# Performance work log

Measured on AMD Instinct MI355X. Metric: run time of the kernel, lower is better.

Reference implementation:

```python
import jax, jax.numpy as jnp
import numpy as np

N_NODES = 100000
N_EDGES = 1600000
IN_CH = 128
HIDDEN = 64
HEADS = 4
C = HIDDEN // HEADS  # per-head channels = 16
NEG_SLOPE = 0.2  # PyG GATConv default leaky_relu slope


def setup_inputs() -> dict:
    key = jax.random.key(0)
    ks = jax.random.split(key, 12)
    x = jax.random.normal(ks[0], (N_NODES, IN_CH), dtype=jnp.float32)
    edge_index = jax.random.randint(ks[1], (2, N_EDGES), 0, N_NODES, dtype=jnp.int64)
    s = 0.1
    params = {
        'w1': jax.random.normal(ks[2], (HIDDEN, IN_CH), dtype=jnp.float32) * s,
        'a_src1': jax.random.normal(ks[3], (HEADS, C), dtype=jnp.float32) * s,
        'a_dst1': jax.random.normal(ks[4], (HEADS, C), dtype=jnp.float32) * s,
        'b1': jax.random.normal(ks[5], (HIDDEN,), dtype=jnp.float32) * s,
        'w2': jax.random.normal(ks[6], (HIDDEN, HIDDEN), dtype=jnp.float32) * s,
        'a_src2': jax.random.normal(ks[7], (HEADS, C), dtype=jnp.float32) * s,
        'a_dst2': jax.random.normal(ks[8], (HEADS, C), dtype=jnp.float32) * s,
        'b2': jax.random.normal(ks[9], (HIDDEN,), dtype=jnp.float32) * s,
        'fc_w': jax.random.normal(ks[10], (1, HIDDEN), dtype=jnp.float32) * s,
        'fc_b': jax.random.normal(ks[11], (1,), dtype=jnp.float32) * s,
    }
    return {'x': x, 'edge_index': edge_index, **params}


def _gat_layer(x, src, dst, W, a_src, a_dst, b):
    # x: [N, F_in]; src/dst: [E'] (self-loops already appended)
    N = x.shape[0]
    h = (x @ W.T).reshape(N, HEADS, C)                      # [N, H, C]
    e_src = jnp.einsum('nhc,hc->nh', h, a_src)              # [N, H]
    e_dst = jnp.einsum('nhc,hc->nh', h, a_dst)              # [N, H]
    alpha = jax.nn.leaky_relu(e_src[src] + e_dst[dst], NEG_SLOPE)  # [E', H]
    # segment softmax over incoming edges of each dst node
    amax = jax.ops.segment_max(alpha, dst, num_segments=N)  # [N, H]
    alpha = jnp.exp(alpha - amax[dst])
    denom = jax.ops.segment_sum(alpha, dst, num_segments=N)
    alpha = alpha / (denom[dst] + 1e-16)
    msg = h[src] * alpha[:, :, None]                        # [E', H, C]
    out = jax.ops.segment_sum(msg, dst, num_segments=N)     # [N, H, C]
    return out.reshape(N, HEADS * C) + b


def _forward(x, edge_index, w1, a_src1, a_dst1, b1, w2, a_src2, a_dst2, b2, fc_w, fc_b):
    N = x.shape[0]
    loops = jnp.arange(N, dtype=edge_index.dtype)
    src = jnp.concatenate([edge_index[0], loops])  # PyG GATConv add_self_loops=True
    dst = jnp.concatenate([edge_index[1], loops])
    x = jax.nn.elu(_gat_layer(x, src, dst, w1, a_src1, a_dst1, b1))
    x = jax.nn.elu(_gat_layer(x, src, dst, w2, a_src2, a_dst2, b2))
    return x @ fc_w.T + fc_b  # [N, 1]


def reference(x, edge_index, w1, a_src1, a_dst1, b1, w2, a_src2, a_dst2, b2, fc_w, fc_b):
    return _forward(x, edge_index, w1, a_src1, a_dst1, b1, w2, a_src2, a_dst2, b2, fc_w, fc_b)
```

## Files before the change

kernel.cpp:

```cpp
#include <hip/hip_runtime.h>
#include <hip/hip_fp16.h>
#include <math.h>

#define NEG_SLOPE 0.2f
#define BSH 8
#define CAPB 6144

__device__ __forceinline__ float lrelu(float x) { return x > 0.f ? x : NEG_SLOPE * x; }

template <typename TIn>
__device__ __forceinline__ float4 ld4(const TIn* p);
template <>
__device__ __forceinline__ float4 ld4<float>(const float* p) { return *(const float4*)p; }
template <>
__device__ __forceinline__ float4 ld4<__half>(const __half* p) {
    uint2 u = *(const uint2*)p;
    union { unsigned v; __half h[2]; } a, b;
    a.v = u.x; b.v = u.y;
    return make_float4(__half2float(a.h[0]), __half2float(a.h[1]),
                       __half2float(b.h[0]), __half2float(b.h[1]));
}

template <int K, typename TIn>
__device__ __forceinline__ void gemm_body(const TIn* __restrict__ x,
                                          const float* __restrict__ W,
                                          const float* __restrict__ a_src,
                                          const float* __restrict__ a_dst,
                                          unsigned short* __restrict__ h_f16,
                                          float* __restrict__ es,
                                          float* __restrict__ ed,
                                          int N, int bid) {
    constexpr int CK = 32;
    __shared__ float xs[CK][68];
    __shared__ float ws[CK][68];
    const int tid = threadIdx.x;
    const int n0 = bid * 64;
    const int tx = tid & 15, ty = tid >> 4;

    float acc[4][4] = {};

    for (int k0 = 0; k0 < K; k0 += CK) {
#pragma unroll
        for (int i = 0; i < 2; ++i) {
            int slot = tid + i * 256;
            int nl = slot >> 3;
            int kq = slot & 7;
            int n = n0 + nl;
            float4 v = (n < N) ? ld4<TIn>(x + (size_t)n * K + k0 + kq * 4)
                               : make_float4(0.f, 0.f, 0.f, 0.f);
            xs[kq * 4 + 0][nl] = v.x; xs[kq * 4 + 1][nl] = v.y;
            xs[kq * 4 + 2][nl] = v.z; xs[kq * 4 + 3][nl] = v.w;
            float4 wv = *(const float4*)(W + (size_t)nl * K + k0 + kq * 4);
            ws[kq * 4 + 0][nl] = wv.x; ws[kq * 4 + 1][nl] = wv.y;
            ws[kq * 4 + 2][nl] = wv.z; ws[kq * 4 + 3][nl] = wv.w;
        }
        __syncthreads();
#pragma unroll
        for (int k = 0; k < CK; ++k) {
            float4 xv = *(const float4*)(&xs[k][ty * 4]);
            float4 wv = *(const float4*)(&ws[k][tx * 4]);
            float xa[4] = {xv.x, xv.y, xv.z, xv.w};
            float wa[4] = {wv.x, wv.y, wv.z, wv.w};
#pragma unroll
            for (int a = 0; a < 4; ++a)
#pragma unroll
                for (int c = 0; c < 4; ++c)
                    acc[a][c] += xa[a] * wa[c];
        }
        __syncthreads();
    }

    const float4 av = *(const float4*)(a_src + tx * 4);
    const float4 dv = *(const float4*)(a_dst + tx * 4);
#pragma unroll
    for (int a = 0; a < 4; ++a) {
        int n = n0 + ty * 4 + a;
        uint2 pk;
        pk.x = (unsigned)__half_as_ushort(__float2half_rn(acc[a][0])) |
               ((unsigned)__half_as_ushort(__float2half_rn(acc[a][1])) << 16);
        pk.y = (unsigned)__half_as_ushort(__float2half_rn(acc[a][2])) |
               ((unsigned)__half_as_ushort(__float2half_rn(acc[a][3])) << 16);
        if (n < N)
            *(uint2*)(h_f16 + (size_t)n * 64 + tx * 4) = pk;
        float e1 = acc[a][0] * av.x + acc[a][1] * av.y + acc[a][2] * av.z + acc[a][3] * av.w;
        float e2 = acc[a][0] * dv.x + acc[a][1] * dv.y + acc[a][2] * dv.z + acc[a][3] * dv.w;
        e1 += __shfl_xor(e1, 1, 64); e2 += __shfl_xor(e2, 1, 64);
        e1 += __shfl_xor(e1, 2, 64); e2 += __shfl_xor(e2, 2, 64);
        if ((tx & 3) == 0 && n < N) {
            es[(size_t)n * 4 + (tx >> 2)] = e1;
            ed[(size_t)n * 4 + (tx >> 2)] = e2;
        }
    }
}

template <int K>
__global__ __launch_bounds__(256) void gemm1_hist(const float* __restrict__ x,
                                                  const float* __restrict__ W,
                                                  const float* __restrict__ a_src,
                                                  const float* __restrict__ a_dst,
                                                  unsigned short* __restrict__ h_f16,
                                                  float* __restrict__ es,
                                                  float* __restrict__ ed, int N,
                                                  const int* __restrict__ dst,
                                                  int* __restrict__ hist_g,
                                                  int E, int Etot, int NBUCK, int nIter,
                                                  int NH) {
    if ((int)blockIdx.x < NH) {
        __shared__ int hist[512];
        int blk = blockIdx.x, tid = threadIdx.x;
        for (int i = tid; i < NBUCK; i += 256) hist[i] = 0;
        __syncthreads();
        int base = blk * nIter * 256;
        for (int i = 0; i < nIter; ++i) {
            int e = base + i * 256 + tid;
            if (e < Etot) {
                int d = (e < E) ? dst[e] : e - E;
                atomicAdd(&hist[d >> BSH], 1);
            }
        }
        __syncthreads();
        for (int i = tid; i < NBUCK; i += 256) hist_g[(size_t)blk * NBUCK + i] = hist[i];
        return;
    }
    gemm_body<K, float>(x, W, a_src, a_dst, h_f16, es, ed, N, blockIdx.x - NH);
}

template <int K, typename TIn>
__global__ __launch_bounds__(256) void gemm_tile(const TIn* __restrict__ x,
                                                 const float* __restrict__ W,
                                                 const float* __restrict__ a_src,
                                                 const float* __restrict__ a_dst,
                                                 unsigned short* __restrict__ h_f16,
                                                 float* __restrict__ es,
                                                 float* __restrict__ ed, int N) {
    gemm_body<K, TIn>(x, W, a_src, a_dst, h_f16, es, ed, N, blockIdx.x);
}

__global__ __launch_bounds__(256) void bucket_scan_blocks(int* __restrict__ hist_g,
                                                          int* __restrict__ tot,
                                                          int NBUCK, int NBLK) {
    __shared__ int s[256];
    int b = blockIdx.x, tid = threadIdx.x;
    int v = (tid < NBLK) ? hist_g[(size_t)tid * NBUCK + b] : 0;
    s[tid] = v; __syncthreads();
#pragma unroll
    for (int off = 1; off < 256; off <<= 1) {
        int t = (tid >= off) ? s[tid - off] : 0;
        __syncthreads();
        s[tid] += t;
        __syncthreads();
    }
    if (tid < NBLK) hist_g[(size_t)tid * NBUCK + b] = s[tid] - v;
    if (tid == 255) tot[b] = s[255];
}

__device__ __forceinline__ void local_tot_scan(const int* __restrict__ tot, int* sv, int NBUCK) {
    int tid = threadIdx.x;
    sv[tid]       = (tid < NBUCK)       ? tot[tid]       : 0;
    sv[tid + 256] = (tid + 256 < NBUCK) ? tot[tid + 256] : 0;
    __syncthreads();
#pragma unroll
    for (int off = 1; off < 512; off <<= 1) {
        int a1 = (tid >= off) ? sv[tid - off] : 0;
        int a2 = (tid + 256 >= off) ? sv[tid + 256 - off] : 0;
        __syncthreads();
        sv[tid] += a1; sv[tid + 256] += a2;
        __syncthreads();
    }
}

__global__ __launch_bounds__(256) void bucket_scatter(const int* __restrict__ src,
                                                      const int* __restrict__ dst,
                                                      const int* __restrict__ hist_g,
                                                      const int* __restrict__ tot,
                                                      unsigned int* __restrict__ bbuf,
                                                      int E, int Etot, int NBUCK, int nIter) {
    __shared__ int sv[512];
    __shared__ int lcur[512];
    int blk = blockIdx.x, tid = threadIdx.x;
    local_tot_scan(tot, sv, NBUCK);
    for (int i = tid; i < NBUCK; i += 256)
        lcur[i] = (sv[i] - tot[i]) + hist_g[(size_t)blk * NBUCK + i];
    __syncthreads();
    int base = blk * nIter * 256;
    for (int i = 0; i < nIter; ++i) {
        int e = base + i * 256 + tid;
        if (e >= Etot) continue;
        int s, d;
        if (e < E) { s = src[e]; d = dst[e]; } else { s = d = e - E; }
        int pos = atomicAdd(&lcur[d >> BSH], 1);
        bbuf[pos] = (unsigned)s | ((unsigned)(d & ((1 << BSH) - 1)) << 24);
    }
}

__global__ __launch_bounds__(256) void bucket_build(const unsigned int* __restrict__ bbuf,
                                                    const int* __restrict__ tot,
                                                    int* __restrict__ col,
                                                    int* __restrict__ offs,
                                                    int N, int NBUCK, int Etot) {
    __shared__ int sv[512];
    __shared__ int cnt[256], lcur[256], s[256];
    __shared__ int ordered[CAPB];
    int b = blockIdx.x, tid = threadIdx.x;
    local_tot_scan(tot, sv, NBUCK);
    const int t  = tot[b];
    const int bb = sv[b] - t;
    const int n0 = b << BSH;
    if (b == 0 && tid == 0) offs[N] = Etot;
    cnt[tid] = 0;
    __syncthreads();
    for (int i = tid; i < t; i += 256) {
        unsigned v = bbuf[bb + i];
        atomicAdd(&cnt[v >> 24], 1);
    }
    __syncthreads();
    int c = cnt[tid];
    s[tid] = c; __syncthreads();
#pragma unroll
    for (int off = 1; off < 256; off <<= 1) {
        int tt = (tid >= off) ? s[tid - off] : 0;
        __syncthreads();
        s[tid] += tt;
        __syncthreads();
    }
    int ex = s[tid] - c;
    lcur[tid] = ex;
    if (n0 + tid < N) offs[n0 + tid] = bb + ex;
    __syncthreads();
    if (t <= CAPB) {
        for (int i = tid; i < t; i += 256) {
            unsigned v = bbuf[bb + i];
            int pos = atomicAdd(&lcur[v >> 24], 1);
            ordered[pos] = (int)(v & 0xFFFFFFu);
        }
        __syncthreads();
        for (int i = tid; i < t; i += 256) col[bb + i] = ordered[i];
    } else {
        for (int i = tid; i < t; i += 256) {
            unsigned v = bbuf[bb + i];
            int pos = atomicAdd(&lcur[v >> 24], 1);
            col[bb + pos] = (int)(v & 0xFFFFFFu);
        }
    }
}

template <bool FINAL>
__global__ __launch_bounds__(256) void gat_gather32(const int* __restrict__ offs,
                                                    const int* __restrict__ col,
                                                    const float* __restrict__ es,
                                                    const float* __restrict__ ed,
                                                    const unsigned short* __restrict__ h_f16,
                                                    const float* __restrict__ b,
                                                    const float* __restrict__ fcw,
                                                    const float* __restrict__ fcb,
                                                    float* __restrict__ xo,
                                                    unsigned short* __restrict__ xo_h,
                                                    int N) {
    int w = (blockIdx.x * 256 + threadIdx.x) >> 6;
    if (w >= N) return;
    const int lane = threadIdx.x & 63;
    const int eslot = lane >> 3, co = lane & 7, hd = co >> 1;
    const int beg = offs[w];
    const int cnt = offs[w + 1] - beg;
    const float edv = ed[(size_t)w * 4 + hd];

    const int cnt64 = min(cnt, 64);
    const int cm1 = cnt64 - 1;
    int myCol = col[beg + min(lane, cm1)];

    int s0 = __shfl(myCol, min(eslot,      cm1), 64);
    int s1 = __shfl(myCol, min(eslot +  8, cm1), 64);
    int s2 = __shfl(myCol, min(eslot + 16, cm1), 64);
    int s3 = __shfl(myCol, min(eslot + 24, cm1), 64);
    float e0 = es[(size_t)s0 * 4 + hd];
    float e1 = es[(size_t)s1 * 4 + hd];
    float e2 = es[(size_t)s2 * 4 + hd];
    float e3 = es[(size_t)s3 * 4 + hd];
    uint4 hv0 = *(const uint4*)(h_f16 + (size_t)s0 * 64 + co * 8);
    uint4 hv1 = *(const uint4*)(h_f16 + (size_t)s1 * 64 + co * 8);
    uint4 hv2 = *(const uint4*)(h_f16 + (size_t)s2 * 64 + co * 8);
    uint4 hv3 = *(const uint4*)(h_f16 + (size_t)s3 * 64 + co * 8);

    float p0 = (eslot      < cnt64) ? __expf(lrelu(e0 + edv)) : 0.f;
    float p1 = (eslot +  8 < cnt64) ? __expf(lrelu(e1 + edv)) : 0.f;
    float p2 = (eslot + 16 < cnt64) ? __expf(lrelu(e2 + edv)) : 0.f;
    float p3 = (eslot + 24 < cnt64) ? __expf(lrelu(e3 + edv)) : 0.f;

    float acc0 = 0.f, acc1 = 0.f, acc2 = 0.f, acc3 = 0.f;
    float acc4 = 0.f, acc5 = 0.f, acc6 = 0.f, acc7 = 0.f;
    float l = (p0 + p1) + (p2 + p3);
    {
        union { uint4 u; __half h[8]; } u0, u1, u2, u3;
        u0.u = hv0; u1.u = hv1; u2.u = hv2; u3.u = hv3;
        acc0 = p0 * __half2float(u0.h[0]) + p1 * __half2float(u1.h[0]) +
               p2 * __half2float(u2.h[0]) + p3 * __half2float(u3.h[0]);
        acc1 = p0 * __half2float(u0.h[1]) + p1 * __half2float(u1.h[1]) +
               p2 * __half2float(u2.h[1]) + p3 * __half2float(u3.h[1]);
        acc2 = p0 * __half2float(u0.h[2]) + p1 * __half2float(u1.h[2]) +
               p2 * __half2float(u2.h[2]) + p3 * __half2float(u3.h[2]);
        acc3 = p0 * __half2float(u0.h[3]) + p1 * __half2float(u1.h[3]) +
               p2 * __half2float(u2.h[3]) + p3 * __half2float(u3.h[3]);
        acc4 = p0 * __half2float(u0.h[4]) + p1 * __half2float(u1.h[4]) +
               p2 * __half2float(u2.h[4]) + p3 * __half2float(u3.h[4]);
        acc5 = p0 * __half2float(u0.h[5]) + p1 * __half2float(u1.h[5]) +
               p2 * __half2float(u2.h[5]) + p3 * __half2float(u3.h[5]);
        acc6 = p0 * __half2float(u0.h[6]) + p1 * __half2float(u1.h[6]) +
               p2 * __half2float(u2.h[6]) + p3 * __half2float(u3.h[6]);
        acc7 = p0 * __half2float(u0.h[7]) + p1 * __half2float(u1.h[7]) +
               p2 * __half2float(u2.h[7]) + p3 * __half2float(u3.h[7]);
    }
    for (int j = 32; j < cnt64; j += 8) {
        int k = j + eslot;
        bool valid = k < cnt64;
        int s = __shfl(myCol, min(k, cm1), 64);
        float a = es[(size_t)s * 4 + hd] + edv;
        float p = valid ? __expf(lrelu(a)) : 0.f;
        union { uint4 u; __half h[8]; } hv;
        hv.u = *(const uint4*)(h_f16 + (size_t)s * 64 + co * 8);
        acc0 += p * __half2float(hv.h[0]); acc1 += p * __half2float(hv.h[1]);
        acc2 += p * __half2float(hv.h[2]); acc3 += p * __half2float(hv.h[3]);
        acc4 += p * __half2float(hv.h[4]); acc5 += p * __half2float(hv.h[5]);
        acc6 += p * __half2float(hv.h[6]); acc7 += p * __half2float(hv.h[7]);
        l += p;
    }
    for (int j = 64; j < cnt; j += 8) {
        int k = j + eslot;
        bool valid = k < cnt;
        int s = valid ? col[beg + k] : 0;
        float a = es[(size_t)s * 4 + hd] + edv;
        float p = valid ? __expf(lrelu(a)) : 0.f;
        union { uint4 u; __half h[8]; } hv;
        hv.u = *(const uint4*)(h_f16 + (size_t)s * 64 + co * 8);
        acc0 += p * __half2float(hv.h[0]); acc1 += p * __half2float(hv.h[1]);
        acc2 += p * __half2float(hv.h[2]); acc3 += p * __half2float(hv.h[3]);
        acc4 += p * __half2float(hv.h[4]); acc5 += p * __half2float(hv.h[5]);
        acc6 += p * __half2float(hv.h[6]); acc7 += p * __half2float(hv.h[7]);
        l += p;
    }
#pragma unroll
    for (int m = 8; m <= 32; m <<= 1) {
        acc0 += __shfl_xor(acc0, m, 64); acc1 += __shfl_xor(acc1, m, 64);
        acc2 += __shfl_xor(acc2, m, 64); acc3 += __shfl_xor(acc3, m, 64);
        acc4 += __shfl_xor(acc4, m, 64); acc5 += __shfl_xor(acc5, m, 64);
        acc6 += __shfl_xor(acc6, m, 64); acc7 += __shfl_xor(acc7, m, 64);
        l    += __shfl_xor(l, m, 64);
    }
    const float inv = 1.f / (l + 1e-16f);
    const float4 bv0 = *(const float4*)(b + co * 8);
    const float4 bv1 = *(const float4*)(b + co * 8 + 4);
    float v0 = acc0 * inv + bv0.x, v1 = acc1 * inv + bv0.y;
    float v2 = acc2 * inv + bv0.z, v3 = acc3 * inv + bv0.w;
    float v4 = acc4 * inv + bv1.x, v5 = acc5 * inv + bv1.y;
    float v6 = acc6 * inv + bv1.z, v7 = acc7 * inv + bv1.w;
    v0 = v0 > 0.f ? v0 : __expf(v0) - 1.f;
    v1 = v1 > 0.f ? v1 : __expf(v1) - 1.f;
    v2 = v2 > 0.f ? v2 : __expf(v2) - 1.f;
    v3 = v3 > 0.f ? v3 : __expf(v3) - 1.f;
    v4 = v4 > 0.f ? v4 : __expf(v4) - 1.f;
    v5 = v5 > 0.f ? v5 : __expf(v5) - 1.f;
    v6 = v6 > 0.f ? v6 : __expf(v6) - 1.f;
    v7 = v7 > 0.f ? v7 : __expf(v7) - 1.f;
    if (FINAL) {
        const float4 fw0 = *(const float4*)(fcw + co * 8);
        const float4 fw1 = *(const float4*)(fcw + co * 8 + 4);
        float t = v0 * fw0.x + v1 * fw0.y + v2 * fw0.z + v3 * fw0.w +
                  v4 * fw1.x + v5 * fw1.y + v6 * fw1.z + v7 * fw1.w;
#pragma unroll
        for (int m = 1; m <= 4; m <<= 1) t += __shfl_xor(t, m, 64);
        if (lane == 0) xo[w] = t + fcb[0];
    } else {
        if (lane < 8) {
            unsigned p0u = (unsigned)__half_as_ushort(__float2half_rn(v0)) |
                           ((unsigned)__half_as_ushort(__float2half_rn(v1)) << 16);
            unsigned p1u = (unsigned)__half_as_ushort(__float2half_rn(v2)) |
                           ((unsigned)__half_as_ushort(__float2half_rn(v3)) << 16);
            unsigned p2u = (unsigned)__half_as_ushort(__float2half_rn(v4)) |
                           ((unsigned)__half_as_ushort(__float2half_rn(v5)) << 16);
            unsigned p3u = (unsigned)__half_as_ushort(__float2half_rn(v6)) |
                           ((unsigned)__half_as_ushort(__float2half_rn(v7)) << 16);
            *(uint4*)(xo_h + (size_t)w * 64 + co * 8) = make_uint4(p0u, p1u, p2u, p3u);
        }
    }
}

extern "C" void kernel_launch(void* const* d_in, const int* in_sizes, int n_in,
                              void* d_out, int out_size, void* d_ws, size_t ws_size,
                              hipStream_t stream) {
    const float* x   = (const float*)d_in[0];
    const int*   ei  = (const int*)d_in[1];
    const float* w1  = (const float*)d_in[2];
    const float* as1 = (const float*)d_in[3];
    const float* ad1 = (const float*)d_in[4];
    const float* b1  = (const float*)d_in[5];
    const float* w2  = (const float*)d_in[6];
    const float* as2 = (const float*)d_in[7];
    const float* ad2 = (const float*)d_in[8];
    const float* b2  = (const float*)d_in[9];
    const float* fcw = (const float*)d_in[10];
    const float* fcb = (const float*)d_in[11];
    float* out = (float*)d_out;

    const int N = in_sizes[0] / 128;
    const int E = in_sizes[1] / 2;
    const int Etot = E + N;
    const int* src = ei;
    const int* dst = ei + E;

    const int NBUCK = (N + 255) >> BSH;
    int CHe = 8192;
    while ((Etot + CHe - 1) / CHe > 256) CHe *= 2;
    const int NBLK = (Etot + CHe - 1) / CHe;
    const int nIter = CHe / 256;

    char* p = (char*)d_ws;
    unsigned short* h_f16 = (unsigned short*)p;  p += (size_t)N * 64 * 2;
    unsigned short* x2    = (unsigned short*)p;  p += (size_t)N * 64 * 2;
    float* es    = (float*)p;  p += (size_t)N * 4 * 4;
    float* ed    = (float*)p;  p += (size_t)N * 4 * 4;
    int* offs    = (int*)p;    p += (size_t)(N + 1) * 4;
    int* tot     = (int*)p;    p += (size_t)NBUCK * 4;
    int* hist_g  = (int*)p;    p += (size_t)NBLK * NBUCK * 4;
    int* col     = (int*)p;    p += (size_t)Etot * 4;
    unsigned int* bbuf = (unsigned int*)p;  p += (size_t)Etot * 4;

    dim3 blk(256);
    const int gN64t = (N + 63) / 64;
    const int gW    = (N * 64 + 255) / 256;

    gemm1_hist<128><<<NBLK + gN64t, blk, 0, stream>>>(x, w1, as1, ad1, h_f16, es, ed, N,
                                                      dst, hist_g, E, Etot, NBUCK, nIter, NBLK);
    bucket_scan_blocks<<<NBUCK, blk, 0, stream>>>(hist_g, tot, NBUCK, NBLK);
    bucket_scatter<<<NBLK, blk, 0, stream>>>(src, dst, hist_g, tot, bbuf, E, Etot, NBUCK, nIter);
    bucket_build<<<NBUCK, blk, 0, stream>>>(bbuf, tot, col, offs, N, NBUCK, Etot);

    gat_gather32<false><<<gW, blk, 0, stream>>>(offs, col, es, ed, h_f16, b1,
                                                nullptr, nullptr, nullptr, x2, N);
    gemm_tile<64, __half><<<gN64t, blk, 0, stream>>>((const __half*)x2, w2, as2, ad2,
                                                     h_f16, es, ed, N);
    gat_gather32<true><<<gW, blk, 0, stream>>>(offs, col, es, ed, h_f16, b2,
                                               fcw, fcb, out, nullptr, N);
}
```

Measured before the change: 187.1 us.

## Replace FP32 SIMT tile GEMMs with fp16 MFMA and LDS-staged epilogue

Both node-projection GEMMs (layer 1 with K=128 fp32 input, layer 2 with K=64 fp16 input) now convert inputs and weights to fp16 in shared memory and use 16x16x32 f16 MFMA instructions instead of FP32 FMA outer products. The epilogue stages the fp16 result through LDS so h can be written with 16-byte stores and attention logits computed per node/head. The goal is to cut compute time in the GEMM phase. The cost is fp16 rounding of x and W before the multiply, plus a larger LDS footprint shared with the histogram path.

Result: faster. 167.4 us (-10.5%).

```diff
diff --git a/kernel.cpp b/kernel.cpp
--- a/kernel.cpp
+++ b/kernel.cpp
@@ -7,89 +7,109 @@
 #define CAPB 6144
 
 __device__ __forceinline__ float lrelu(float x) { return x > 0.f ? x : NEG_SLOPE * x; }
+
+using half4 = __attribute__((ext_vector_type(4))) _Float16;
+using half8 = __attribute__((ext_vector_type(8))) _Float16;
+using f32x4 = __attribute__((ext_vector_type(4))) float;
 
 template <typename TIn>
 __device__ __forceinline__ float4 ld4(const TIn* p);
 template <>
 __device__ __forceinline__ float4 ld4<float>(const float* p) { return *(const float4*)p; }
 template <>
-__device__ __forceinline__ float4 ld4<__half>(const __half* p) {
-    uint2 u = *(const uint2*)p;
-    union { unsigned v; __half h[2]; } a, b;
-    a.v = u.x; b.v = u.y;
-    return make_float4(__half2float(a.h[0]), __half2float(a.h[1]),
-                       __half2float(b.h[0]), __half2float(b.h[1]));
+__device__ __forceinline__ float4 ld4<_Float16>(const _Float16* p) {
+    half4 v = *(const half4*)p;
+    return make_float4((float)v[0], (float)v[1], (float)v[2], (float)v[3]);
 }
 
 template <int K, typename TIn>
-__device__ __forceinline__ void gemm_body(const TIn* __restrict__ x,
-                                          const float* __restrict__ W,
-                                          const float* __restrict__ a_src,
-                                          const float* __restrict__ a_dst,
-                                          unsigned short* __restrict__ h_f16,
-                                          float* __restrict__ es,
-                                          float* __restrict__ ed,
-                                          int N, int bid) {
-    constexpr int CK = 32;
-    __shared__ float xs[CK][68];
-    __shared__ float ws[CK][68];
+__device__ __forceinline__ void gemm_mfma_body(const TIn* __restrict__ x,
+                                               const float* __restrict__ W,
+                                               const float* __restrict__ a_src,
+                                               const float* __restrict__ a_dst,
+                                               unsigned short* __restrict__ h_f16,
+                                               float* __restrict__ es,
+                                               float* __restrict__ ed,
+                                               int N, int bid, _Float16* sm) {
+    constexpr int KP = K + 8;
+    _Float16* xs = sm;
+    _Float16* ws = sm + 64 * KP;
     const int tid = threadIdx.x;
     const int n0 = bid * 64;
-    const int tx = tid & 15, ty = tid >> 4;
-
-    float acc[4][4] = {};
-
-    for (int k0 = 0; k0 < K; k0 += CK) {
-#pragma unroll
-        for (int i = 0; i < 2; ++i) {
-            int slot = tid + i * 256;
-            int nl = slot >> 3;
-            int kq = slot & 7;
-            int n = n0 + nl;
-            float4 v = (n < N) ? ld4<TIn>(x + (size_t)n * K + k0 + kq * 4)
-                               : make_float4(0.f, 0.f, 0.f, 0.f);
-            xs[kq * 4 + 0][nl] = v.x; xs[kq * 4 + 1][nl] = v.y;
-            xs[kq * 4 + 2][nl] = v.z; xs[kq * 4 + 3][nl] = v.w;
-            float4 wv = *(const float4*)(W + (size_t)nl * K + k0 + kq * 4);
-            ws[kq * 4 + 0][nl] = wv.x; ws[kq * 4 + 1][nl] = wv.y;
-            ws[kq * 4 + 2][nl] = wv.z; ws[kq * 4 + 3][nl] = wv.w;
+
+    constexpr int KV = K / 4;
+    for (int idx = tid; idx < 64 * KV; idx += 256) {
+        int r = idx / KV, kq = idx - r * KV;
+        int n = n0 + r;
+        float4 v = (n < N) ? ld4<TIn>(x + (size_t)n * K + kq * 4)
+                           : make_float4(0.f, 0.f, 0.f, 0.f);
+        half4 hv = {(_Float16)v.x, (_Float16)v.y, (_Float16)v.z, (_Float16)v.w};
+        *(half4*)&xs[r * KP + kq * 4] = hv;
+        float4 wv = *(const float4*)(W + (size_t)r * K + kq * 4);
+        half4 wh = {(_Float16)wv.x, (_Float16)wv.y, (_Float16)wv.z, (_Float16)wv.w};
+        *(half4*)&ws[r * KP + kq * 4] = wh;
+    }
+    __syncthreads();
+
+    const int wv_ = tid >> 6, lane = tid & 63;
+    const int lrow = lane & 15, g = lane >> 4;
+    f32x4 acc0 = {0.f, 0.f, 0.f, 0.f}, acc1 = acc0, acc2 = acc0, acc3 = acc0;
+#pragma unroll
+    for (int ks = 0; ks < K / 32; ++ks) {
+        const int ko = ks * 32 + g * 8;
+        half8 af = *(const half8*)&xs[(wv_ * 16 + lrow) * KP + ko];
+        half8 b0 = *(const half8*)&ws[(lrow) * KP + ko];
+        half8 b1 = *(const half8*)&ws[(16 + lrow) * KP + ko];
+        half8 b2 = *(const half8*)&ws[(32 + lrow) * KP + ko];
+        half8 b3 = *(const half8*)&ws[(48 + lrow) * KP + ko];
+        acc0 = __builtin_amdgcn_mfma_f32_16x16x32_f16(af, b0, acc0, 0, 0, 0);
+        acc1 = __builtin_amdgcn_mfma_f32_16x16x32_f16(af, b1, acc1, 0, 0, 0);
+        acc2 = __builtin_amdgcn_mfma_f32_16x16x32_f16(af, b2, acc2, 0, 0, 0);
+        acc3 = __builtin_amdgcn_mfma_f32_16x16x32_f16(af, b3, acc3, 0, 0, 0);
+    }
+    __syncthreads();
+
+    _Float16* ht = sm;
+#pragma unroll
+    for (int reg = 0; reg < 4; ++reg) {
+        int r = wv_ * 16 + g * 4 + reg;
+        ht[r * 72 +      lrow] = (_Float16)acc0[reg];
+        ht[r * 72 + 16 + lrow] = (_Float16)acc1[reg];
+        ht[r * 72 + 32 + lrow] = (_Float16)acc2[reg];
+        ht[r * 72 + 48 + lrow] = (_Float16)acc3[reg];
+    }
+    __syncthreads();
+
+    {
+        int nl = tid >> 2, hd = tid & 3;
+        half8 hA = *(const half8*)&ht[nl * 72 + hd * 16];
+        half8 hB = *(const half8*)&ht[nl * 72 + hd * 16 + 8];
+        const float4 s0 = *(const float4*)(a_src + hd * 16);
+        const float4 s1 = *(const float4*)(a_src + hd * 16 + 4);
+        const float4 s2 = *(const float4*)(a_src + hd * 16 + 8);
+        const float4 s3 = *(const float4*)(a_src + hd * 16 + 12);
+        const float4 d0 = *(const float4*)(a_dst + hd * 16);
+        const float4 d1 = *(const float4*)(a_dst + hd * 16 + 4);
+        const float4 d2 = *(const float4*)(a_dst + hd * 16 + 8);
+        const float4 d3 = *(const float4*)(a_dst + hd * 16 + 12);
+        float e1 = (float)hA[0]*s0.x + (float)hA[1]*s0.y + (float)hA[2]*s0.z + (float)hA[3]*s0.w
+                 + (float)hA[4]*s1.x + (float)hA[5]*s1.y + (float)hA[6]*s1.z + (float)hA[7]*s1.w
+                 + (float)hB[0]*s2.x + (float)hB[1]*s2.y + (float)hB[2]*s2.z + (float)hB[3]*s2.w
+                 + (float)hB[4]*s3.x + (float)hB[5]*s3.y + (float)hB[6]*s3.z + (float)hB[7]*s3.w;
+        float e2 = (float)hA[0]*d0.x + (float)hA[1]*d0.y + (float)hA[2]*d0.z + (float)hA[3]*d0.w
+                 + (float)hA[4]*d1.x + (float)hA[5]*d1.y + (float)hA[6]*d1.z + (float)hA[7]*d1.w
+                 + (float)hB[0]*d2.x + (float)hB[1]*d2.y + (float)hB[2]*d2.z + (float)hB[3]*d2.w
+                 + (float)hB[4]*d3.x + (float)hB[5]*d3.y + (float)hB[6]*d3.z + (float)hB[7]*d3.w;
+        int n = n0 + nl;
+        if (n < N) {
+            es[(size_t)n * 4 + hd] = e1;
+            ed[(size_t)n * 4 + hd] = e2;
         }
-        __syncthreads();
-#pragma unroll
-        for (int k = 0; k < CK; ++k) {
-            float4 xv = *(const float4*)(&xs[k][ty * 4]);
-            float4 wv = *(const float4*)(&ws[k][tx * 4]);
-            float xa[4] = {xv.x, xv.y, xv.z, xv.w};
-            float wa[4] = {wv.x, wv.y, wv.z, wv.w};
-#pragma unroll
-            for (int a = 0; a < 4; ++a)
-#pragma unroll
-                for (int c = 0; c < 4; ++c)
-                    acc[a][c] += xa[a] * wa[c];
-        }
-        __syncthreads();
-    }
-
-    const float4 av = *(const float4*)(a_src + tx * 4);
-    const float4 dv = *(const float4*)(a_dst + tx * 4);
-#pragma unroll
-    for (int a = 0; a < 4; ++a) {
-        int n = n0 + ty * 4 + a;
-        uint2 pk;
-        pk.x = (unsigned)__half_as_ushort(__float2half_rn(acc[a][0])) |
-               ((unsigned)__half_as_ushort(__float2half_rn(acc[a][1])) << 16);
-        pk.y = (unsigned)__half_as_ushort(__float2half_rn(acc[a][2])) |
-               ((unsigned)__half_as_ushort(__float2half_rn(acc[a][3])) << 16);
-        if (n < N)
-            *(uint2*)(h_f16 + (size_t)n * 64 + tx * 4) = pk;
-        float e1 = acc[a][0] * av.x + acc[a][1] * av.y + acc[a][2] * av.z + acc[a][3] * av.w;
-        float e2 = acc[a][0] * dv.x + acc[a][1] * dv.y + acc[a][2] * dv.z + acc[a][3] * dv.w;
-        e1 += __shfl_xor(e1, 1, 64); e2 += __shfl_xor(e2, 1, 64);
-        e1 += __shfl_xor(e1, 2, 64); e2 += __shfl_xor(e2, 2, 64);
-        if ((tx & 3) == 0 && n < N) {
-            es[(size_t)n * 4 + (tx >> 2)] = e1;
-            ed[(size_t)n * 4 + (tx >> 2)] = e2;
-        }
+    }
+    for (int idx = tid; idx < 512; idx += 256) {
+        int r = idx >> 3, c8 = (idx & 7) << 3;
+        if (n0 + r < N)
+            *(uint4*)(h_f16 + (size_t)(n0 + r) * 64 + c8) = *(const uint4*)&ht[r * 72 + c8];
     }
 }
 
@@ -105,8 +125,9 @@
                                                   int* __restrict__ hist_g,
                                                   int E, int Etot, int NBUCK, int nIter,
                                                   int NH) {
+    __shared__ _Float16 sm[2 * 64 * (K + 8)];
     if ((int)blockIdx.x < NH) {
-        __shared__ int hist[512];
+        int* hist = (int*)sm;
         int blk = blockIdx.x, tid = threadIdx.x;
         for (int i = tid; i < NBUCK; i += 256) hist[i] = 0;
         __syncthreads();
@@ -122,18 +143,19 @@
         for (int i = tid; i < NBUCK; i += 256) hist_g[(size_t)blk * NBUCK + i] = hist[i];
         return;
     }
-    gemm_body<K, float>(x, W, a_src, a_dst, h_f16, es, ed, N, blockIdx.x - NH);
+    gemm_mfma_body<K, float>(x, W, a_src, a_dst, h_f16, es, ed, N, blockIdx.x - NH, sm);
 }
 
 template <int K, typename TIn>
-__global__ __launch_bounds__(256) void gemm_tile(const TIn* __restrict__ x,
+__global__ __launch_bounds__(256) void gemm_mfma(const TIn* __restrict__ x,
                                                  const float* __restrict__ W,
                                                  const float* __restrict__ a_src,
                                                  const float* __restrict__ a_dst,
                                                  unsigned short* __restrict__ h_f16,
                                                  float* __restrict__ es,
                                                  float* __restrict__ ed, int N) {
-    gemm_body<K, TIn>(x, W, a_src, a_dst, h_f16, es, ed, N, blockIdx.x);
+    __shared__ _Float16 sm[2 * 64 * (K + 8)];
+    gemm_mfma_body<K, TIn>(x, W, a_src, a_dst, h_f16, es, ed, N, blockIdx.x, sm);
 }
 
 __global__ __launch_bounds__(256) void bucket_scan_blocks(int* __restrict__ hist_g,
@@ -435,8 +457,8 @@
 
     gat_gather32<false><<<gW, blk, 0, stream>>>(offs, col, es, ed, h_f16, b1,
                                                 nullptr, nullptr, nullptr, x2, N);
-    gemm_tile<64, __half><<<gN64t, blk, 0, stream>>>((const __half*)x2, w2, as2, ad2,
-                                                     h_f16, es, ed, N);
+    gemm_mfma<64, _Float16><<<gN64t, blk, 0, stream>>>((const _Float16*)x2, w2, as2, ad2,
+                                                       h_f16, es, ed, N);
     gat_gather32<true><<<gW, blk, 0, stream>>>(offs, col, es, ed, h_f16, b2,
                                                fcw, fcb, out, nullptr, N);
 }
```
